# Kernel optimization log

Measured on AMD Instinct MI355X. Metric: run time of the kernel, lower is better.

## Reference

```python
import jax, jax.numpy as jnp
import numpy as np

B, S, HID = 4, 4096, 2048
H, NB = 16, 4
D = HID // H
EPS = 1e-6

def elu_plus_one(x):
    return jax.nn.elu(x) + 1.0

def setup_inputs() -> dict:
    key = jax.random.key(0)
    ks = jax.random.split(key, 8)
    return {
        "hidden_states": jax.random.normal(ks[0], (B, S, HID), jnp.float32),
        "Wq": jax.random.normal(ks[1], (HID, HID), jnp.float32) * 0.02,
        "Wk": jax.random.normal(ks[2], (HID, HID), jnp.float32) * 0.02,
        "Wv": jax.random.normal(ks[3], (HID, HID), jnp.float32) * 0.02,
        "Wo": jax.random.normal(ks[4], (HID, HID), jnp.float32) * 0.02,
        "bank_weights": jax.random.normal(ks[5], (H, NB), jnp.float32) * 0.02,
        "memories": jax.random.uniform(ks[6], (NB, H, D, D), jnp.float32),
        "memory_norms": jax.random.uniform(ks[7], (NB, H, D), jnp.float32),
    }

def reference(hidden_states, Wq, Wk, Wv, Wo, bank_weights, memories, memory_norms):
    b, s, _ = hidden_states.shape
    # projections (torch Linear: x @ W.T), reshape to [B,H,S,D]
    def proj(W):
        return (hidden_states @ W.T).reshape(b, s, H, D).transpose(0, 2, 1, 3)
    q, k, v = proj(Wq), proj(Wk), proj(Wv)

    # ---- retrieve from all banks (vectorized over bank dim n) ----
    sigma_q = elu_plus_one(q)                                     # [B,H,S,D]
    a_unnorm = jnp.einsum('bhsd,nhde->nbhse', sigma_q, memories)  # [NB,B,H,S,D]
    norm = jnp.einsum('bhsd,nhd->nbhs', sigma_q, memory_norms)
    a = a_unnorm / jnp.clip(norm, EPS, None)[..., None]
    # banks with (near-)zero norm contribute zeros (torch early-return)
    active = (memory_norms.sum(axis=(1, 2)) >= EPS).astype(a.dtype)  # [NB]
    a = a * active[:, None, None, None, None]
    weights = jax.nn.softmax(bank_weights, axis=-1)               # [H,NB]
    combined = jnp.einsum('nbhse,hn->bhse', a, weights)           # [B,H,S,D]

    # ---- delta-rule update of current bank (bank 0) ----
    sigma_k = elu_plus_one(k)
    mem0, norm0 = memories[0], memory_norms[0]
    retr = jnp.einsum('bhsd,hde->bhse', sigma_k, mem0)
    knorm = jnp.clip(jnp.einsum('bhsd,hd->bhs', sigma_k, norm0), EPS, None)
    delta_v = v - retr / knorm[..., None]
    mem_update = jnp.einsum('bhsd,bhse->hde', sigma_k, delta_v) / (b * s)
    new_mem0 = jax.lax.stop_gradient(mem0 + mem_update)
    new_norm0 = jax.lax.stop_gradient(norm0 + sigma_k.sum(axis=(0, 2)) / b)

    out = combined.transpose(0, 2, 1, 3).reshape(b, s, HID) @ Wo.T
    return out, new_mem0, new_norm0
```

## Files before the change

### kernel.cpp

```cpp
#include <hip/hip_runtime.h>
#include <cstdint>
#include <cstddef>

#define NTOK 16384
#define HIDN 2048
#define NH   16
#define HD   128
#define NB   4
#define EPSF 1e-6f

typedef __attribute__((ext_vector_type(8))) short bvec8;
typedef __attribute__((ext_vector_type(4))) float fvec4;

__device__ __forceinline__ unsigned short f2bf(float x) {
  union { float f; uint32_t u; } v; v.f = x;
  uint32_t r = (v.u + 0x7fffu + ((v.u >> 16) & 1u)) >> 16;
  return (unsigned short)r;
}
__device__ __forceinline__ float bf2f(unsigned short b) {
  union { uint32_t u; float f; } v; v.u = ((uint32_t)b) << 16;
  return v.f;
}
__device__ __forceinline__ float elu1(float x) { return x > 0.f ? x + 1.f : __expf(x); }

__global__ void prep_kernel(const float* __restrict__ bw, const float* __restrict__ mnorm,
                            float* __restrict__ wact) {
  __shared__ float act[NB];
  int tid = threadIdx.x;
  if (tid < NB) {
    float s = 0.f;
    for (int i = 0; i < NH * HD; i++) s += mnorm[tid * NH * HD + i];
    act[tid] = (s >= EPSF) ? 1.f : 0.f;
  }
  __syncthreads();
  int h = tid >> 2, n = tid & 3;
  float w0 = bw[h*4+0], w1 = bw[h*4+1], w2 = bw[h*4+2], w3 = bw[h*4+3];
  float mx = fmaxf(fmaxf(w0, w1), fmaxf(w2, w3));
  float e0 = __expf(w0-mx), e1 = __expf(w1-mx), e2 = __expf(w2-mx), e3 = __expf(w3-mx);
  float sum = e0 + e1 + e2 + e3;
  float en = (n == 0) ? e0 : ((n == 1) ? e1 : ((n == 2) ? e2 : e3));
  wact[tid] = (en / sum) * act[n];
}

__global__ __launch_bounds__(256) void cast_bf16_kernel(const float* __restrict__ src,
                                                        unsigned short* __restrict__ dst, int n8) {
  int i = blockIdx.x * 256 + threadIdx.x;
  if (i >= n8) return;
  const float4* s = (const float4*)src + (size_t)i * 2;
  float4 a = s[0], b = s[1];
  uint32_t p0 = (uint32_t)f2bf(a.x) | ((uint32_t)f2bf(a.y) << 16);
  uint32_t p1 = (uint32_t)f2bf(a.z) | ((uint32_t)f2bf(a.w) << 16);
  uint32_t p2 = (uint32_t)f2bf(b.x) | ((uint32_t)f2bf(b.y) << 16);
  uint32_t p3 = (uint32_t)f2bf(b.z) | ((uint32_t)f2bf(b.w) << 16);
  uint4 o; o.x = p0; o.y = p1; o.z = p2; o.w = p3;
  *(uint4*)(dst + (size_t)i * 8) = o;
}

__global__ __launch_bounds__(256) void mem_transpose_kernel(const float* __restrict__ mem,
                                                            unsigned short* __restrict__ membT) {
  int nh = blockIdx.x;
  const float* src = mem + (size_t)nh * (HD * HD);
  unsigned short* dst = membT + (size_t)nh * (HD * HD);
  for (int i = threadIdx.x; i < HD * HD; i += 256) {
    int d = i >> 7, e = i & 127;
    dst[e * HD + d] = f2bf(src[i]);
  }
}

template<int MODE>
__global__ __launch_bounds__(256) void gemm_nt_kernel(
    const unsigned short* __restrict__ A, const unsigned short* __restrict__ B,
    int K, int N,
    unsigned short* __restrict__ oq, unsigned short* __restrict__ ok,
    unsigned short* __restrict__ ov, float* __restrict__ oc) {
  __shared__ unsigned short As[128 * 40];
  __shared__ unsigned short Bs[128 * 40];
  const int tid = threadIdx.x;
  const int wave = tid >> 6, lane = tid & 63;
  const int lr = lane & 15, lq = lane >> 4;
  const int wr = (wave >> 1) * 64, wc = (wave & 1) * 64;
  const int bm = blockIdx.x, bn = blockIdx.y;
  const size_t arow0 = (size_t)bm * 128;
  const size_t brow0 = (size_t)bn * 128;
  fvec4 acc[4][4] = {};
  for (int k0 = 0; k0 < K; k0 += 32) {
    __syncthreads();
#pragma unroll
    for (int p = 0; p < 2; p++) {
      int c = tid + p * 256;
      int row = c >> 2, kc = (c & 3) * 8;
      *(uint4*)(As + row * 40 + kc) = *(const uint4*)(A + (arow0 + row) * K + k0 + kc);
      *(uint4*)(Bs + row * 40 + kc) = *(const uint4*)(B + (brow0 + row) * K + k0 + kc);
    }
    __syncthreads();
    bvec8 af[4], bfr[4];
#pragma unroll
    for (int mi = 0; mi < 4; mi++)
      af[mi] = *(const bvec8*)(As + (wr + mi * 16 + lr) * 40 + lq * 8);
#pragma unroll
    for (int ni = 0; ni < 4; ni++)
      bfr[ni] = *(const bvec8*)(Bs + (wc + ni * 16 + lr) * 40 + lq * 8);
#pragma unroll
    for (int mi = 0; mi < 4; mi++)
#pragma unroll
      for (int ni = 0; ni < 4; ni++)
        acc[mi][ni] = __builtin_amdgcn_mfma_f32_16x16x32_bf16(af[mi], bfr[ni], acc[mi][ni], 0, 0, 0);
  }
#pragma unroll
  for (int mi = 0; mi < 4; mi++) {
#pragma unroll
    for (int ni = 0; ni < 4; ni++) {
#pragma unroll
      for (int r = 0; r < 4; r++) {
        int grow = bm * 128 + wr + mi * 16 + lq * 4 + r;
        int gcol = bn * 128 + wc + ni * 16 + lr;
        float v = acc[mi][ni][r];
        if (MODE == 0) {
          int seg = gcol >> 11;
          int col = gcol & 2047;
          unsigned short* dst = (seg == 0) ? oq : ((seg == 1) ? ok : ov);
          float t = (seg < 2) ? elu1(v) : v;
          dst[(size_t)grow * HIDN + col] = f2bf(t);
        } else {
          oc[(size_t)grow * N + gcol] = v;
        }
      }
    }
  }
}

__global__ __launch_bounds__(256) void coeff_kernel(
    const unsigned short* __restrict__ sq, const unsigned short* __restrict__ sk,
    const float* __restrict__ mnorm, const float* __restrict__ wact,
    float* __restrict__ cbuf, float* __restrict__ knorm) {
  int g = blockIdx.x * 256 + threadIdx.x;
  int t = g >> 4, h = g & 15;
  const unsigned short* qp = sq + (size_t)t * HIDN + h * HD;
  const unsigned short* kp = sk + (size_t)t * HIDN + h * HD;
  const float* m0 = mnorm + (0 * NH + h) * HD;
  const float* m1 = mnorm + (1 * NH + h) * HD;
  const float* m2 = mnorm + (2 * NH + h) * HD;
  const float* m3 = mnorm + (3 * NH + h) * HD;
  float n0 = 0, n1 = 0, n2 = 0, n3 = 0, kn = 0;
  for (int i = 0; i < HD; i++) {
    float qv = bf2f(qp[i]);
    float kv = bf2f(kp[i]);
    n0 += qv * m0[i]; n1 += qv * m1[i]; n2 += qv * m2[i]; n3 += qv * m3[i];
    kn += kv * m0[i];
  }
  cbuf[(size_t)g * 4 + 0] = wact[h * 4 + 0] / fmaxf(n0, EPSF);
  cbuf[(size_t)g * 4 + 1] = wact[h * 4 + 1] / fmaxf(n1, EPSF);
  cbuf[(size_t)g * 4 + 2] = wact[h * 4 + 2] / fmaxf(n2, EPSF);
  cbuf[(size_t)g * 4 + 3] = wact[h * 4 + 3] / fmaxf(n3, EPSF);
  knorm[g] = fmaxf(kn, EPSF);
}

__global__ __launch_bounds__(256) void retrieve_kernel(
    const unsigned short* __restrict__ sq, const unsigned short* __restrict__ membT,
    const float* __restrict__ cbuf, unsigned short* __restrict__ comb) {
  __shared__ unsigned short Sq[64 * 136];
  __shared__ unsigned short Mt[128 * 136];
  __shared__ float ct[64 * 4];
  const int tb = blockIdx.x, h = blockIdx.y;
  const int tid = threadIdx.x;
  const int wave = tid >> 6, lane = tid & 63;
  const int lr = lane & 15, lq = lane >> 4;
  const int wr = (wave >> 1) * 32, wc = (wave & 1) * 64;
#pragma unroll
  for (int p = 0; p < 4; p++) {
    int c = tid + p * 256;
    int row = c >> 4, col = (c & 15) * 8;
    *(uint4*)(Sq + row * 136 + col) =
        *(const uint4*)(sq + (size_t)(tb * 64 + row) * HIDN + h * HD + col);
  }
  {
    int tl = tid >> 2, n = tid & 3;
    ct[tid] = cbuf[(((size_t)(tb * 64 + tl)) * NH + h) * 4 + n];
  }
  float wacc[2][4][4] = {};
  for (int n = 0; n < NB; n++) {
    __syncthreads();
    const unsigned short* msrc = membT + (size_t)(n * NH + h) * (HD * HD);
#pragma unroll
    for (int p = 0; p < 8; p++) {
      int c = tid + p * 256;
      int row = c >> 4, col = (c & 15) * 8;
      *(uint4*)(Mt + row * 136 + col) = *(const uint4*)(msrc + row * HD + col);
    }
    __syncthreads();
    fvec4 u[2][4] = {};
#pragma unroll
    for (int dk = 0; dk < HD; dk += 32) {
      bvec8 af[2], bfr[4];
#pragma unroll
      for (int mi = 0; mi < 2; mi++)
        af[mi] = *(const bvec8*)(Sq + (wr + mi * 16 + lr) * 136 + dk + lq * 8);
#pragma unroll
      for (int ni = 0; ni < 4; ni++)
        bfr[ni] = *(const bvec8*)(Mt + (wc + ni * 16 + lr) * 136 + dk + lq * 8);
#pragma unroll
      for (int mi = 0; mi < 2; mi++)
#pragma unroll
        for (int ni = 0; ni < 4; ni++)
          u[mi][ni] = __builtin_amdgcn_mfma_f32_16x16x32_bf16(af[mi], bfr[ni], u[mi][ni], 0, 0, 0);
    }
#pragma unroll
    for (int mi = 0; mi < 2; mi++)
#pragma unroll
      for (int ni = 0; ni < 4; ni++)
#pragma unroll
        for (int r = 0; r < 4; r++) {
          int rl = wr + mi * 16 + lq * 4 + r;
          wacc[mi][ni][r] += ct[rl * 4 + n] * u[mi][ni][r];
        }
  }
#pragma unroll
  for (int mi = 0; mi < 2; mi++)
#pragma unroll
    for (int ni = 0; ni < 4; ni++)
#pragma unroll
      for (int r = 0; r < 4; r++) {
        int rl = wr + mi * 16 + lq * 4 + r;
        int col = h * HD + wc + ni * 16 + lr;
        comb[(size_t)(tb * 64 + rl) * HIDN + col] = f2bf(wacc[mi][ni][r]);
      }
}

__global__ __launch_bounds__(256) void delta_kernel(
    const unsigned short* __restrict__ sk, const unsigned short* __restrict__ membT,
    const unsigned short* __restrict__ vb, const float* __restrict__ knorm,
    unsigned short* __restrict__ dv) {
  __shared__ unsigned short Sk[64 * 136];
  __shared__ unsigned short Mt[128 * 136];
  const int tb = blockIdx.x, h = blockIdx.y;
  const int tid = threadIdx.x;
  const int wave = tid >> 6, lane = tid & 63;
  const int lr = lane & 15, lq = lane >> 4;
  const int wr = (wave >> 1) * 32, wc = (wave & 1) * 64;
#pragma unroll
  for (int p = 0; p < 4; p++) {
    int c = tid + p * 256;
    int row = c >> 4, col = (c & 15) * 8;
    *(uint4*)(Sk + row * 136 + col) =
        *(const uint4*)(sk + (size_t)(tb * 64 + row) * HIDN + h * HD + col);
  }
  const unsigned short* msrc = membT + (size_t)h * (HD * HD);
#pragma unroll
  for (int p = 0; p < 8; p++) {
    int c = tid + p * 256;
    int row = c >> 4, col = (c & 15) * 8;
    *(uint4*)(Mt + row * 136 + col) = *(const uint4*)(msrc + row * HD + col);
  }
  __syncthreads();
  fvec4 u[2][4] = {};
#pragma unroll
  for (int dk = 0; dk < HD; dk += 32) {
    bvec8 af[2], bfr[4];
#pragma unroll
    for (int mi = 0; mi < 2; mi++)
      af[mi] = *(const bvec8*)(Sk + (wr + mi * 16 + lr) * 136 + dk + lq * 8);
#pragma unroll
    for (int ni = 0; ni < 4; ni++)
      bfr[ni] = *(const bvec8*)(Mt + (wc + ni * 16 + lr) * 136 + dk + lq * 8);
#pragma unroll
    for (int mi = 0; mi < 2; mi++)
#pragma unroll
      for (int ni = 0; ni < 4; ni++)
        u[mi][ni] = __builtin_amdgcn_mfma_f32_16x16x32_bf16(af[mi], bfr[ni], u[mi][ni], 0, 0, 0);
  }
#pragma unroll
  for (int mi = 0; mi < 2; mi++)
#pragma unroll
    for (int ni = 0; ni < 4; ni++)
#pragma unroll
      for (int r = 0; r < 4; r++) {
        int rl = wr + mi * 16 + lq * 4 + r;
        int t = tb * 64 + rl;
        int e = wc + ni * 16 + lr;
        float kn = knorm[(size_t)t * NH + h];
        float vv = bf2f(vb[(size_t)t * HIDN + h * HD + e]);
        dv[(size_t)t * HIDN + h * HD + e] = f2bf(vv - u[mi][ni][r] / kn);
      }
}

__global__ __launch_bounds__(256) void memupd_kernel(const unsigned short* __restrict__ sk,
                                                     const unsigned short* __restrict__ dv,
                                                     float* __restrict__ upd) {
  const int h = blockIdx.x, kc = blockIdx.y;
  __shared__ float sA[8][128], sB[8][128];
  const int tid = threadIdx.x;
  const int tr = tid >> 4, tc = tid & 15;
  float acc[8][8] = {};
  for (int t0 = kc * 512; t0 < kc * 512 + 512; t0 += 8) {
    __syncthreads();
    int row = tid >> 5, col = (tid & 31) * 4;
    const unsigned short* ap = sk + (size_t)(t0 + row) * HIDN + h * HD + col;
    const unsigned short* bp = dv + (size_t)(t0 + row) * HIDN + h * HD + col;
    ushort4 av = *(const ushort4*)ap;
    ushort4 bv = *(const ushort4*)bp;
    sA[row][col + 0] = bf2f(av.x); sA[row][col + 1] = bf2f(av.y);
    sA[row][col + 2] = bf2f(av.z); sA[row][col + 3] = bf2f(av.w);
    sB[row][col + 0] = bf2f(bv.x); sB[row][col + 1] = bf2f(bv.y);
    sB[row][col + 2] = bf2f(bv.z); sB[row][col + 3] = bf2f(bv.w);
    __syncthreads();
#pragma unroll
    for (int tt = 0; tt < 8; tt++) {
      float a[8], b[8];
#pragma unroll
      for (int i = 0; i < 8; i++) a[i] = sA[tt][tr * 8 + i];
#pragma unroll
      for (int j = 0; j < 8; j++) b[j] = sB[tt][tc * 8 + j];
#pragma unroll
      for (int i = 0; i < 8; i++)
#pragma unroll
        for (int j = 0; j < 8; j++) acc[i][j] += a[i] * b[j];
    }
  }
#pragma unroll
  for (int i = 0; i < 8; i++)
#pragma unroll
    for (int j = 0; j < 8; j++)
      atomicAdd(&upd[((size_t)h * HD + tr * 8 + i) * HD + tc * 8 + j], acc[i][j]);
}

__global__ __launch_bounds__(256) void colsum_kernel(const unsigned short* __restrict__ sk,
                                                     float* __restrict__ colsum) {
  int b = blockIdx.x;
  int tid = threadIdx.x;
  float acc[8] = {};
  for (int t = b * 64; t < b * 64 + 64; t++) {
    const unsigned short* p = sk + (size_t)t * HIDN;
#pragma unroll
    for (int j = 0; j < 8; j++) acc[j] += bf2f(p[tid + j * 256]);
  }
#pragma unroll
  for (int j = 0; j < 8; j++) atomicAdd(&colsum[tid + j * 256], acc[j]);
}

__global__ __launch_bounds__(256) void finalize_kernel(
    const float* __restrict__ mem, const float* __restrict__ mnorm,
    const float* __restrict__ upd, const float* __restrict__ colsum,
    float* __restrict__ out_mem, float* __restrict__ out_norm) {
  int i = blockIdx.x * 256 + threadIdx.x;
  if (i < NH * HD * HD) out_mem[i] = mem[i] + upd[i] * (1.f / 16384.f);
  if (i < HIDN) out_norm[i] = mnorm[i] + colsum[i] * 0.25f;
}

extern "C" void kernel_launch(void* const* d_in, const int* in_sizes, int n_in,
                              void* d_out, int out_size, void* d_ws, size_t ws_size,
                              hipStream_t stream) {
  (void)in_sizes; (void)n_in; (void)out_size; (void)ws_size;
  const float* hidden = (const float*)d_in[0];
  const float* Wq = (const float*)d_in[1];
  const float* Wk = (const float*)d_in[2];
  const float* Wv = (const float*)d_in[3];
  const float* Wo = (const float*)d_in[4];
  const float* bw = (const float*)d_in[5];
  const float* mem = (const float*)d_in[6];
  const float* mnorm = (const float*)d_in[7];

  float* out = (float*)d_out;
  float* out_mem = out + (size_t)NTOK * HIDN;
  float* out_norm = out_mem + NH * HD * HD;

  char* w = (char*)d_ws;
  size_t off = 0;
  auto alloc = [&](size_t bytes) {
    char* p = w + off;
    off += (bytes + 255) & ~(size_t)255;
    return p;
  };
  unsigned short* Xb    = (unsigned short*)alloc((size_t)NTOK * HIDN * 2);
  unsigned short* Wqkvb = (unsigned short*)alloc((size_t)3 * HIDN * HIDN * 2);
  unsigned short* Wob   = (unsigned short*)alloc((size_t)HIDN * HIDN * 2);
  unsigned short* sq    = (unsigned short*)alloc((size_t)NTOK * HIDN * 2);
  unsigned short* sk    = (unsigned short*)alloc((size_t)NTOK * HIDN * 2);
  unsigned short* vb    = (unsigned short*)alloc((size_t)NTOK * HIDN * 2);
  unsigned short* dvb   = (unsigned short*)alloc((size_t)NTOK * HIDN * 2);
  float* cbuf   = (float*)alloc((size_t)NTOK * NH * 4 * 4);
  float* knorm  = (float*)alloc((size_t)NTOK * NH * 4);
  float* wact   = (float*)alloc(256);
  unsigned short* membT = (unsigned short*)alloc((size_t)NB * NH * HD * HD * 2);
  float* upd    = (float*)alloc((size_t)NH * HD * HD * 4);
  float* colsum = (float*)alloc(HIDN * 4);
  unsigned short* comb = Xb;

  (void)hipMemsetAsync(upd, 0, (size_t)NH * HD * HD * 4, stream);
  (void)hipMemsetAsync(colsum, 0, HIDN * 4, stream);

  prep_kernel<<<1, 64, 0, stream>>>(bw, mnorm, wact);
  cast_bf16_kernel<<<NTOK * HIDN / 8 / 256, 256, 0, stream>>>(hidden, Xb, NTOK * HIDN / 8);
  cast_bf16_kernel<<<HIDN * HIDN / 8 / 256, 256, 0, stream>>>(Wq, Wqkvb, HIDN * HIDN / 8);
  cast_bf16_kernel<<<HIDN * HIDN / 8 / 256, 256, 0, stream>>>(Wk, Wqkvb + (size_t)HIDN * HIDN, HIDN * HIDN / 8);
  cast_bf16_kernel<<<HIDN * HIDN / 8 / 256, 256, 0, stream>>>(Wv, Wqkvb + (size_t)2 * HIDN * HIDN, HIDN * HIDN / 8);
  cast_bf16_kernel<<<HIDN * HIDN / 8 / 256, 256, 0, stream>>>(Wo, Wob, HIDN * HIDN / 8);
  mem_transpose_kernel<<<NB * NH, 256, 0, stream>>>(mem, membT);

  gemm_nt_kernel<0><<<dim3(NTOK / 128, 3 * HIDN / 128), 256, 0, stream>>>(
      Xb, Wqkvb, HIDN, 3 * HIDN, sq, sk, vb, nullptr);

  coeff_kernel<<<NTOK * NH / 256, 256, 0, stream>>>(sq, sk, mnorm, wact, cbuf, knorm);
  retrieve_kernel<<<dim3(NTOK / 64, NH), 256, 0, stream>>>(sq, membT, cbuf, comb);
  delta_kernel<<<dim3(NTOK / 64, NH), 256, 0, stream>>>(sk, membT, vb, knorm, dvb);
  memupd_kernel<<<dim3(NH, 32), 256, 0, stream>>>(sk, dvb, upd);
  colsum_kernel<<<NTOK / 64, 256, 0, stream>>>(sk, colsum);
  finalize_kernel<<<NH * HD * HD / 256, 256, 0, stream>>>(mem, mnorm, upd, colsum, out_mem, out_norm);

  gemm_nt_kernel<1><<<dim3(NTOK / 128, HIDN / 128), 256, 0, stream>>>(
      comb, Wob, HIDN, HIDN, nullptr, nullptr, nullptr, out);
}
```

Baseline: 1.894 ms.

## Use direct global-to-LDS loads with unpadded chunked tiles; parallelize prep and coeff

Staging of GEMM, retrieve and delta tiles into shared memory now uses the global_load_lds builtin with 16-byte transfers. Data goes straight from global memory to LDS without passing through registers. To fit the lane-contiguous write pattern this requires, the LDS tiles drop their row padding and are stored as contiguous 32-column k-chunks. Separately, the prep kernel's bank-norm sum is split across all threads with shared atomics, and the coeff kernel reads 16-byte vectors instead of scalar bf16 values. The unpadded layout may add LDS bank conflicts on the MFMA fragment reads.

```diff
diff --git a/kernel.cpp b/kernel.cpp
--- a/kernel.cpp
+++ b/kernel.cpp
@@ -12,6 +12,11 @@
 typedef __attribute__((ext_vector_type(8))) short bvec8;
 typedef __attribute__((ext_vector_type(4))) float fvec4;
 
+#define GLOAD_LDS16(gp, lp)                                                     \
+  __builtin_amdgcn_global_load_lds(                                             \
+      (const __attribute__((address_space(1))) void*)(gp),                      \
+      (__attribute__((address_space(3))) void*)(lp), 16, 0, 0)
+
 __device__ __forceinline__ unsigned short f2bf(float x) {
   union { float f; uint32_t u; } v; v.f = x;
   uint32_t r = (v.u + 0x7fffu + ((v.u >> 16) & 1u)) >> 16;
@@ -25,12 +30,15 @@
 
 __global__ void prep_kernel(const float* __restrict__ bw, const float* __restrict__ mnorm,
                             float* __restrict__ wact) {
-  __shared__ float act[NB];
+  __shared__ float acc[NB];
   int tid = threadIdx.x;
-  if (tid < NB) {
+  if (tid < NB) acc[tid] = 0.f;
+  __syncthreads();
+  {
+    int n = tid & 3, part = tid >> 2;
     float s = 0.f;
-    for (int i = 0; i < NH * HD; i++) s += mnorm[tid * NH * HD + i];
-    act[tid] = (s >= EPSF) ? 1.f : 0.f;
+    for (int i = part; i < NH * HD; i += 16) s += mnorm[n * NH * HD + i];
+    atomicAdd(&acc[n], s);
   }
   __syncthreads();
   int h = tid >> 2, n = tid & 3;
@@ -39,7 +47,8 @@
   float e0 = __expf(w0-mx), e1 = __expf(w1-mx), e2 = __expf(w2-mx), e3 = __expf(w3-mx);
   float sum = e0 + e1 + e2 + e3;
   float en = (n == 0) ? e0 : ((n == 1) ? e1 : ((n == 2) ? e2 : e3));
-  wact[tid] = (en / sum) * act[n];
+  float act = (acc[n] >= EPSF) ? 1.f : 0.f;
+  wact[tid] = (en / sum) * act;
 }
 
 __global__ __launch_bounds__(256) void cast_bf16_kernel(const float* __restrict__ src,
@@ -73,8 +82,8 @@
     int K, int N,
     unsigned short* __restrict__ oq, unsigned short* __restrict__ ok,
     unsigned short* __restrict__ ov, float* __restrict__ oc) {
-  __shared__ unsigned short As[128 * 40];
-  __shared__ unsigned short Bs[128 * 40];
+  __shared__ __align__(16) unsigned short As[128 * 32];
+  __shared__ __align__(16) unsigned short Bs[128 * 32];
   const int tid = threadIdx.x;
   const int wave = tid >> 6, lane = tid & 63;
   const int lr = lane & 15, lq = lane >> 4;
@@ -87,19 +96,20 @@
     __syncthreads();
 #pragma unroll
     for (int p = 0; p < 2; p++) {
-      int c = tid + p * 256;
-      int row = c >> 2, kc = (c & 3) * 8;
-      *(uint4*)(As + row * 40 + kc) = *(const uint4*)(A + (arow0 + row) * K + k0 + kc);
-      *(uint4*)(Bs + row * 40 + kc) = *(const uint4*)(B + (brow0 + row) * K + k0 + kc);
+      int c = p * 256 + tid;
+      int row = c >> 2, j = c & 3;
+      int cb = __builtin_amdgcn_readfirstlane(c);
+      GLOAD_LDS16(A + (arow0 + row) * K + k0 + j * 8, As + (size_t)cb * 8);
+      GLOAD_LDS16(B + (brow0 + row) * K + k0 + j * 8, Bs + (size_t)cb * 8);
     }
     __syncthreads();
     bvec8 af[4], bfr[4];
 #pragma unroll
     for (int mi = 0; mi < 4; mi++)
-      af[mi] = *(const bvec8*)(As + (wr + mi * 16 + lr) * 40 + lq * 8);
+      af[mi] = *(const bvec8*)(As + (wr + mi * 16 + lr) * 32 + lq * 8);
 #pragma unroll
     for (int ni = 0; ni < 4; ni++)
-      bfr[ni] = *(const bvec8*)(Bs + (wc + ni * 16 + lr) * 40 + lq * 8);
+      bfr[ni] = *(const bvec8*)(Bs + (wc + ni * 16 + lr) * 32 + lq * 8);
 #pragma unroll
     for (int mi = 0; mi < 4; mi++)
 #pragma unroll
@@ -142,11 +152,25 @@
   const float* m2 = mnorm + (2 * NH + h) * HD;
   const float* m3 = mnorm + (3 * NH + h) * HD;
   float n0 = 0, n1 = 0, n2 = 0, n3 = 0, kn = 0;
-  for (int i = 0; i < HD; i++) {
-    float qv = bf2f(qp[i]);
-    float kv = bf2f(kp[i]);
-    n0 += qv * m0[i]; n1 += qv * m1[i]; n2 += qv * m2[i]; n3 += qv * m3[i];
-    kn += kv * m0[i];
+#pragma unroll 4
+  for (int i = 0; i < HD; i += 8) {
+    uint4 qv4 = *(const uint4*)(qp + i);
+    uint4 kv4 = *(const uint4*)(kp + i);
+    const uint32_t qw[4] = {qv4.x, qv4.y, qv4.z, qv4.w};
+    const uint32_t kw[4] = {kv4.x, kv4.y, kv4.z, kv4.w};
+#pragma unroll
+    for (int j = 0; j < 4; j++) {
+      float q0 = bf2f((unsigned short)(qw[j] & 0xffff));
+      float q1 = bf2f((unsigned short)(qw[j] >> 16));
+      float k0 = bf2f((unsigned short)(kw[j] & 0xffff));
+      float k1 = bf2f((unsigned short)(kw[j] >> 16));
+      int i0 = i + j * 2, i1 = i + j * 2 + 1;
+      n0 += q0 * m0[i0] + q1 * m0[i1];
+      n1 += q0 * m1[i0] + q1 * m1[i1];
+      n2 += q0 * m2[i0] + q1 * m2[i1];
+      n3 += q0 * m3[i0] + q1 * m3[i1];
+      kn += k0 * m0[i0] + k1 * m0[i1];
+    }
   }
   cbuf[(size_t)g * 4 + 0] = wact[h * 4 + 0] / fmaxf(n0, EPSF);
   cbuf[(size_t)g * 4 + 1] = wact[h * 4 + 1] / fmaxf(n1, EPSF);
@@ -158,8 +182,8 @@
 __global__ __launch_bounds__(256) void retrieve_kernel(
     const unsigned short* __restrict__ sq, const unsigned short* __restrict__ membT,
     const float* __restrict__ cbuf, unsigned short* __restrict__ comb) {
-  __shared__ unsigned short Sq[64 * 136];
-  __shared__ unsigned short Mt[128 * 136];
+  __shared__ __align__(16) unsigned short Sq[4 * 64 * 32];
+  __shared__ __align__(16) unsigned short Mt[4 * 128 * 32];
   __shared__ float ct[64 * 4];
   const int tb = blockIdx.x, h = blockIdx.y;
   const int tid = threadIdx.x;
@@ -168,10 +192,11 @@
   const int wr = (wave >> 1) * 32, wc = (wave & 1) * 64;
 #pragma unroll
   for (int p = 0; p < 4; p++) {
-    int c = tid + p * 256;
-    int row = c >> 4, col = (c & 15) * 8;
-    *(uint4*)(Sq + row * 136 + col) =
-        *(const uint4*)(sq + (size_t)(tb * 64 + row) * HIDN + h * HD + col);
+    int c = p * 256 + tid;
+    int kc = c >> 8, r = (c >> 2) & 63, j = c & 3;
+    int cb = __builtin_amdgcn_readfirstlane(c);
+    GLOAD_LDS16(sq + (size_t)(tb * 64 + r) * HIDN + h * HD + kc * 32 + j * 8,
+                Sq + (size_t)cb * 8);
   }
   {
     int tl = tid >> 2, n = tid & 3;
@@ -183,21 +208,23 @@
     const unsigned short* msrc = membT + (size_t)(n * NH + h) * (HD * HD);
 #pragma unroll
     for (int p = 0; p < 8; p++) {
-      int c = tid + p * 256;
-      int row = c >> 4, col = (c & 15) * 8;
-      *(uint4*)(Mt + row * 136 + col) = *(const uint4*)(msrc + row * HD + col);
+      int c = p * 256 + tid;
+      int kc = c >> 9, r = (c >> 2) & 127, j = c & 3;
+      int cb = __builtin_amdgcn_readfirstlane(c);
+      GLOAD_LDS16(msrc + r * HD + kc * 32 + j * 8, Mt + (size_t)cb * 8);
     }
     __syncthreads();
     fvec4 u[2][4] = {};
 #pragma unroll
     for (int dk = 0; dk < HD; dk += 32) {
+      int kc = dk >> 5;
       bvec8 af[2], bfr[4];
 #pragma unroll
       for (int mi = 0; mi < 2; mi++)
-        af[mi] = *(const bvec8*)(Sq + (wr + mi * 16 + lr) * 136 + dk + lq * 8);
+        af[mi] = *(const bvec8*)(Sq + (kc * 64 + wr + mi * 16 + lr) * 32 + lq * 8);
 #pragma unroll
       for (int ni = 0; ni < 4; ni++)
-        bfr[ni] = *(const bvec8*)(Mt + (wc + ni * 16 + lr) * 136 + dk + lq * 8);
+        bfr[ni] = *(const bvec8*)(Mt + (kc * 128 + wc + ni * 16 + lr) * 32 + lq * 8);
 #pragma unroll
       for (int mi = 0; mi < 2; mi++)
 #pragma unroll
@@ -230,8 +257,8 @@
     const unsigned short* __restrict__ sk, const unsigned short* __restrict__ membT,
     const unsigned short* __restrict__ vb, const float* __restrict__ knorm,
     unsigned short* __restrict__ dv) {
-  __shared__ unsigned short Sk[64 * 136];
-  __shared__ unsigned short Mt[128 * 136];
+  __shared__ __align__(16) unsigned short Sk[4 * 64 * 32];
+  __shared__ __align__(16) unsigned short Mt[4 * 128 * 32];
   const int tb = blockIdx.x, h = blockIdx.y;
   const int tid = threadIdx.x;
   const int wave = tid >> 6, lane = tid & 63;
@@ -239,29 +266,32 @@
   const int wr = (wave >> 1) * 32, wc = (wave & 1) * 64;
 #pragma unroll
   for (int p = 0; p < 4; p++) {
-    int c = tid + p * 256;
-    int row = c >> 4, col = (c & 15) * 8;
-    *(uint4*)(Sk + row * 136 + col) =
-        *(const uint4*)(sk + (size_t)(tb * 64 + row) * HIDN + h * HD + col);
+    int c = p * 256 + tid;
+    int kc = c >> 8, r = (c >> 2) & 63, j = c & 3;
+    int cb = __builtin_amdgcn_readfirstlane(c);
+    GLOAD_LDS16(sk + (size_t)(tb * 64 + r) * HIDN + h * HD + kc * 32 + j * 8,
+                Sk + (size_t)cb * 8);
   }
   const unsigned short* msrc = membT + (size_t)h * (HD * HD);
 #pragma unroll
   for (int p = 0; p < 8; p++) {
-    int c = tid + p * 256;
-    int row = c >> 4, col = (c & 15) * 8;
-    *(uint4*)(Mt + row * 136 + col) = *(const uint4*)(msrc + row * HD + col);
+    int c = p * 256 + tid;
+    int kc = c >> 9, r = (c >> 2) & 127, j = c & 3;
+    int cb = __builtin_amdgcn_readfirstlane(c);
+    GLOAD_LDS16(msrc + r * HD + kc * 32 + j * 8, Mt + (size_t)cb * 8);
   }
   __syncthreads();
   fvec4 u[2][4] = {};
 #pragma unroll
   for (int dk = 0; dk < HD; dk += 32) {
+    int kc = dk >> 5;
     bvec8 af[2], bfr[4];
 #pragma unroll
     for (int mi = 0; mi < 2; mi++)
-      af[mi] = *(const bvec8*)(Sk + (wr + mi * 16 + lr) * 136 + dk + lq * 8);
+      af[mi] = *(const bvec8*)(Sk + (kc * 64 + wr + mi * 16 + lr) * 32 + lq * 8);
 #pragma unroll
     for (int ni = 0; ni < 4; ni++)
-      bfr[ni] = *(const bvec8*)(Mt + (wc + ni * 16 + lr) * 136 + dk + lq * 8);
+      bfr[ni] = *(const bvec8*)(Mt + (kc * 128 + wc + ni * 16 + lr) * 32 + lq * 8);
 #pragma unroll
     for (int mi = 0; mi < 2; mi++)
 #pragma unroll
```

New measurement: 1.603 ms. 15.4% less time.
